# Performance work log

Measured on AMD Instinct MI355X. Metric: run time of the kernel, lower is better.

Reference implementation:

```python
import jax, jax.numpy as jnp
import numpy as np

NEG_SLOPE = 0.2


def setup_inputs() -> dict:
    key = jax.random.key(0)
    ks = jax.random.split(key, 7)
    N, E, IN, H, D = 100000, 1000000, 256, 4, 32
    feat = jax.random.normal(ks[0], (N, IN), dtype=jnp.float32)
    W_fc = jax.random.normal(ks[1], (H * D, IN), dtype=jnp.float32) * (1.0 / np.sqrt(IN))
    attn_l = jax.random.normal(ks[2], (1, H, D), dtype=jnp.float32) * 0.1
    attn_r = jax.random.normal(ks[3], (1, H, D), dtype=jnp.float32) * 0.1
    bias = jnp.zeros((H * D,), dtype=jnp.float32)
    src = jax.random.randint(ks[4], (E,), 0, N, dtype=jnp.int32)
    dst = jax.random.randint(ks[5], (E,), 0, N, dtype=jnp.int32)
    return {"feat": feat, "W_fc": W_fc, "attn_l": attn_l, "attn_r": attn_r, "bias": bias, "src": src, "dst": dst}


def reference(feat, W_fc, attn_l, attn_r, bias, src, dst):
    N = feat.shape[0]
    H, D = attn_l.shape[1], attn_l.shape[2]
    # fc projection; note: in the non-tuple path the module uses self.fc for
    # BOTH feat_src and feat_src2, so they are identical.
    h = (feat @ W_fc.T).reshape(N, H, D)  # [N,H,D]
    el = jnp.sum(h * attn_l, axis=-1)  # [N,H]
    er = jnpp_sum = jnp.sum(h * attn_r, axis=-1)  # [N,H]
    e = jax.nn.leaky_relu(el[src] + er[dst], NEG_SLOPE)  # [E,H]
    # edge softmax normalized over incoming edges of each dst node
    e_max = jax.ops.segment_max(e, dst, num_segments=N)  # [N,H]
    ex = jnp.exp(e - e_max[dst])
    denom = jax.ops.segment_sum(ex, dst, num_segments=N)  # [N,H]
    a = ex / denom[dst]  # [E,H]
    # attention-weighted aggregation: sum_e a_e * h[src_e] -> dst
    initial_ft = jax.ops.segment_sum(h[src] * a[:, :, None], dst, num_segments=N)
    # second path: u_mul_v then sum to dst (feat_src2 == feat_dst2 == h)
    add_ft = jax.ops.segment_sum(h[src] * h[dst], dst, num_segments=N)
    rst = initial_ft + add_ft + bias.reshape(1, H, D)
    return rst
```

## Files before the change

### kernel.cpp

```cpp
#include <hip/hip_runtime.h>
#include <hip/hip_bf16.h>
#include <hip/hip_fp16.h>
#include <math.h>

#define NEG_SLOPE 0.2f

typedef __attribute__((ext_vector_type(8))) short short8v;
typedef __attribute__((ext_vector_type(4))) float f32x4;

__device__ __forceinline__ float uas(unsigned int u) { return __uint_as_float(u); }

__device__ __forceinline__ unsigned short f2bf(float x) {
    __hip_bfloat16 b = __float2bfloat16(x);
    return *(unsigned short*)&b;
}

#define NPB_SHIFT 8
#define BCAP_SHIFT 13
#define BCAP (1 << BCAP_SHIFT)
#define BIN_EDGES 2048
#define BS_EPT    4
#define GEMM_BLOCKS 512

__global__ void k_prep(const float* __restrict__ W, const float* __restrict__ al,
                       const float* __restrict__ ar, short* __restrict__ wfrag,
                       int* __restrict__ bcur, int NB, int* __restrict__ tilectr) {
    int p = blockIdx.x * 256 + threadIdx.x;
    if (p < NB) bcur[p] = p << BCAP_SHIFT;
    if (p == 0) *tilectr = 0;
    if (p >= 144 * 32) return;
    int n = p >> 5, kg = p & 31;
    float v[8];
    if (n < 128) {
        const float* wp = W + (size_t)n * 256 + kg * 8;
        float4 v0 = *(const float4*)wp;
        float4 v1 = *(const float4*)(wp + 4);
        v[0] = v0.x; v[1] = v0.y; v[2] = v0.z; v[3] = v0.w;
        v[4] = v1.x; v[5] = v1.y; v[6] = v1.z; v[7] = v1.w;
    } else if (n < 136) {
        int i = n - 128, hh = i & 3, lr = i >> 2;
        const float* av = lr ? ar : al;
#pragma unroll
        for (int j = 0; j < 8; j++) v[j] = 0.f;
        for (int c = 0; c < 32; c++) {
            float a = av[hh * 32 + c];
            const float* wp = W + (size_t)(hh * 32 + c) * 256 + kg * 8;
#pragma unroll
            for (int j = 0; j < 8; j++) v[j] += a * wp[j];
        }
    } else {
#pragma unroll
        for (int j = 0; j < 8; j++) v[j] = 0.f;
    }
    short s8[8];
#pragma unroll
    for (int j = 0; j < 8; j++) s8[j] = (short)f2bf(v[j]);
    int kstep = kg >> 2, ntile = n >> 4;
    int L     = (kg & 3) * 16 + (n & 15);
    int slot  = kstep * 9 + ntile;
    *(short8v*)&wfrag[(slot * 64 + L) * 8] = *(short8v*)s8;
}

__global__ __launch_bounds__(512, 4) void k_gemm(const float* __restrict__ feat,
                                                 const short* __restrict__ wfrag,
                                                 unsigned short* __restrict__ hb,
                                                 float* __restrict__ el,
                                                 float* __restrict__ er, int N,
                                                 int ntiles,
                                                 int* __restrict__ tilectr) {
    __shared__ short wlds[36864];
    __shared__ int tsh;
    const int t    = threadIdx.x;
    const int lane = t & 63;
    const int wave = t >> 6;
    const int g    = lane >> 4;
    const int c    = lane & 15;

#pragma unroll
    for (int i = 0; i < 9; i++) {
        int p = t + i * 512;
        *(short8v*)&wlds[(size_t)p * 8] = *(const short8v*)&wfrag[(size_t)p * 8];
    }
    __syncthreads();

    for (;;) {
        if (t == 0) tsh = atomicAdd(tilectr, 1);
        __syncthreads();
        const int tile = tsh;
        __syncthreads();
        if (tile >= ntiles) break;

        const int n0  = tile * 128;
        const int row = n0 + wave * 16 + c;
        const int rc  = row < N ? row : N - 1;
        const float* ap = feat + (size_t)rc * 256 + g * 8;

        float4 a4[16];
#pragma unroll
        for (int ks = 0; ks < 8; ks++) {
            a4[2 * ks]     = *(const float4*)(ap + ks * 32);
            a4[2 * ks + 1] = *(const float4*)(ap + ks * 32 + 4);
        }

        f32x4 acc[9];
#pragma unroll
        for (int nt = 0; nt < 9; nt++) acc[nt] = (f32x4){0.f, 0.f, 0.f, 0.f};

#pragma unroll
        for (int ks = 0; ks < 8; ks++) {
            float4 v0 = a4[2 * ks], v1 = a4[2 * ks + 1];
            short s8[8];
            s8[0] = (short)f2bf(v0.x); s8[1] = (short)f2bf(v0.y);
            s8[2] = (short)f2bf(v0.z); s8[3] = (short)f2bf(v0.w);
            s8[4] = (short)f2bf(v1.x); s8[5] = (short)f2bf(v1.y);
            s8[6] = (short)f2bf(v1.z); s8[7] = (short)f2bf(v1.w);
            short8v afrag = *(short8v*)s8;
#pragma unroll
            for (int nt = 0; nt < 9; nt++) {
                short8v b = *(short8v*)&wlds[(((size_t)ks * 9 + nt) * 64 + lane) * 8];
                acc[nt] = __builtin_amdgcn_mfma_f32_16x16x32_bf16(afrag, b, acc[nt], 0, 0, 0);
            }
        }

#pragma unroll
        for (int r = 0; r < 4; r++) {
            int m = n0 + wave * 16 + g * 4 + r;
            if (m < N) {
#pragma unroll
                for (int nt = 0; nt < 8; nt++)
                    hb[(size_t)m * 128 + nt * 16 + c] = f2bf(acc[nt][r]);
                float av = acc[8][r];
                if (c < 4)      el[(size_t)m * 4 + c]       = av;
                else if (c < 8) er[(size_t)m * 4 + (c - 4)] = av;
            }
        }
    }
}

__global__ __launch_bounds__(512) void k_binscatter(const int* __restrict__ src,
                                                    const int* __restrict__ dst,
                                                    int* __restrict__ bcur,
                                                    unsigned int* __restrict__ binned,
                                                    int E, int NB) {
    __shared__ int hist[512];
    __shared__ int scn[512];
    __shared__ int lcur[512];
    __shared__ int gdelta[512];
    __shared__ int ebuf[BIN_EDGES];
    __shared__ int dbuf[BIN_EDGES];
    int t = threadIdx.x;
    hist[t] = 0;
    __syncthreads();
    int wbase = blockIdx.x * BIN_EDGES;
    int base  = wbase + t;
    int ne    = E - wbase; if (ne > BIN_EDGES) ne = BIN_EDGES;
    int sv[BS_EPT], dv[BS_EPT];
#pragma unroll
    for (int k = 0; k < BS_EPT; k++) {
        int idx = base + k * 512;
        if (idx < E) {
            sv[k] = src[idx];
            dv[k] = dst[idx];
            atomicAdd(&hist[dv[k] >> NPB_SHIFT], 1);
        } else {
            dv[k] = -1;
        }
    }
    __syncthreads();
    scn[t] = hist[t];
    __syncthreads();
    for (int off = 1; off < 512; off <<= 1) {
        int v = (t >= off) ? scn[t - off] : 0;
        __syncthreads();
        scn[t] += v;
        __syncthreads();
    }
    if (t < NB) {
        int h  = hist[t];
        int lb = scn[t] - h;
        int g  = h ? atomicAdd(&bcur[t], h) : 0;
        gdelta[t] = g - lb;
        lcur[t]   = lb;
    }
    __syncthreads();
#pragma unroll
    for (int k = 0; k < BS_EPT; k++) {
        if (dv[k] >= 0) {
            int bkt  = dv[k] >> NPB_SHIFT;
            int slot = atomicAdd(&lcur[bkt], 1);
            ebuf[slot] = sv[k];
            dbuf[slot] = dv[k];
        }
    }
    __syncthreads();
    for (int j = t; j < ne; j += 512) {
        int d = dbuf[j];
        binned[j + gdelta[d >> NPB_SHIFT]] =
            (unsigned int)ebuf[j] | ((unsigned int)(d & 255) << 24);
    }
}

__global__ __launch_bounds__(512) void k_csr(const unsigned int* __restrict__ binned,
                                             const int* __restrict__ bcur,
                                             int* __restrict__ startA,
                                             int* __restrict__ deg,
                                             int* __restrict__ src_csr, int N) {
    __shared__ int hist[256];
    __shared__ int scn[256];
    __shared__ int cur[256];
    __shared__ int sbuf[4096];
    int b = blockIdx.x;
    int t = threadIdx.x;
    int base = b << BCAP_SHIFT;
    int cnt  = bcur[b] - base;
    int node0 = b << NPB_SHIFT;
    if (t < 256) hist[t] = 0;
    __syncthreads();
    for (int i = t; i < cnt; i += 512) {
        unsigned int e = binned[base + i];
        atomicAdd(&hist[e >> 24], 1);
    }
    __syncthreads();
    int h = (t < 256) ? hist[t] : 0;
    if (t < 256) scn[t] = h;
    __syncthreads();
    for (int off = 1; off < 256; off <<= 1) {
        int v = (t < 256 && t >= off) ? scn[t - off] : 0;
        __syncthreads();
        if (t < 256) scn[t] += v;
        __syncthreads();
    }
    if (t < 256) {
        int excl  = scn[t] - h;
        int gnode = node0 + t;
        if (gnode < N) { startA[gnode] = base + excl; deg[gnode] = h; }
        cur[t] = excl;
    }
    __syncthreads();
    if (cnt <= 4096) {
        for (int i = t; i < cnt; i += 512) {
            unsigned int e = binned[base + i];
            int p = atomicAdd(&cur[e >> 24], 1);
            sbuf[p] = (int)(e & 0xFFFFFFu);
        }
        __syncthreads();
        for (int i = t; i < cnt; i += 512)
            src_csr[base + i] = sbuf[i];
    } else {
        for (int i = t; i < cnt; i += 512) {
            unsigned int e = binned[base + i];
            int p = atomicAdd(&cur[e >> 24], 1);
            src_csr[base + p] = (int)(e & 0xFFFFFFu);
        }
    }
}

__global__ __launch_bounds__(256) void k_agg(
        const unsigned int* __restrict__ hbu,
        const float* __restrict__ el, const float* __restrict__ er,
        const int* __restrict__ src_csr, const int* __restrict__ start,
        const int* __restrict__ deg,
        const float* __restrict__ bias, float* __restrict__ out, int N) {
    int wid  = blockIdx.x * 4 + (threadIdx.x >> 6);
    int lane = threadIdx.x & 63;
    if (wid >= N) return;
    int beg = __builtin_amdgcn_readfirstlane(start[wid]);
    int dg  = __builtin_amdgcn_readfirstlane(deg[wid]);
    int head = lane >> 4;

    float er_own = er[(size_t)wid * 4 + head];
    unsigned int uh = hbu[(size_t)wid * 64 + lane];
    float2 bv = ((const float2*)bias)[lane];

    float S1x = 0.f, S1y = 0.f, S2x = 0.f, S2y = 0.f, dd = 0.f;
    int i = 0;
    for (; i + 8 <= dg; i += 8) {
        int b = beg + i;
        int s[8];
#pragma unroll
        for (int k = 0; k < 8; k++) s[k] = src_csr[b + k];
        unsigned int u[8];
#pragma unroll
        for (int k = 0; k < 8; k++) u[k] = hbu[(size_t)s[k] * 64 + lane];
        float ev[8];
#pragma unroll
        for (int k = 0; k < 8; k++) ev[k] = el[(size_t)s[k] * 4 + head];
#pragma unroll
        for (int k = 0; k < 8; k++) {
            float tt = ev[k] + er_own;
            tt = fmaxf(tt, NEG_SLOPE * tt);
            float w = __expf(tt);
            float x = uas(u[k] << 16), y = uas(u[k] & 0xFFFF0000u);
            S1x += x; S1y += y;
            S2x += w * x; S2y += w * y;
            dd  += w;
        }
    }
    for (; i + 4 <= dg; i += 4) {
        int b = beg + i;
        int s[4];
#pragma unroll
        for (int k = 0; k < 4; k++) s[k] = src_csr[b + k];
        unsigned int u[4];
#pragma unroll
        for (int k = 0; k < 4; k++) u[k] = hbu[(size_t)s[k] * 64 + lane];
        float ev[4];
#pragma unroll
        for (int k = 0; k < 4; k++) ev[k] = el[(size_t)s[k] * 4 + head];
#pragma unroll
        for (int k = 0; k < 4; k++) {
            float tt = ev[k] + er_own;
            tt = fmaxf(tt, NEG_SLOPE * tt);
            float w = __expf(tt);
            float x = uas(u[k] << 16), y = uas(u[k] & 0xFFFF0000u);
            S1x += x; S1y += y;
            S2x += w * x; S2y += w * y;
            dd  += w;
        }
    }
    for (; i < dg; i++) {
        int s0 = src_csr[beg + i];
        unsigned int u0 = hbu[(size_t)s0 * 64 + lane];
        float tt = el[(size_t)s0 * 4 + head] + er_own;
        tt = fmaxf(tt, NEG_SLOPE * tt);
        float w0 = __expf(tt);
        float x0 = uas(u0 << 16), y0 = uas(u0 & 0xFFFF0000u);
        S1x += x0; S1y += y0;
        S2x += w0 * x0; S2y += w0 * y0;
        dd  += w0;
    }

    float hvx = uas(uh << 16), hvy = uas(uh & 0xFFFF0000u);
    float inv = dd > 0.f ? 1.f / dd : 0.f;
    float ox = bv.x + hvx * S1x + S2x * inv;
    float oy = bv.y + hvy * S1y + S2y * inv;
    float2 o = {ox, oy};
    ((float2*)(out + (size_t)wid * 128))[lane] = o;
}

extern "C" void kernel_launch(void* const* d_in, const int* in_sizes, int n_in,
                              void* d_out, int out_size, void* d_ws, size_t ws_size,
                              hipStream_t stream) {
    const float* feat = (const float*)d_in[0];
    const float* W_fc = (const float*)d_in[1];
    const float* al   = (const float*)d_in[2];
    const float* ar   = (const float*)d_in[3];
    const float* bias = (const float*)d_in[4];
    const int*   src  = (const int*)d_in[5];
    const int*   dst  = (const int*)d_in[6];
    const int N = in_sizes[0] / 256;
    const int E = in_sizes[5];
    const int NB = (N + 255) >> NPB_SHIFT;

    char* ws = (char*)d_ws;
    size_t off = 0;
    unsigned int* hbu = (unsigned int*)(ws + off); off += (size_t)N * 64 * 4;
    float* el         = (float*)(ws + off); off += (size_t)N * 4 * 4;
    float* er         = (float*)(ws + off); off += (size_t)N * 4 * 4;
    int* startA       = (int*)(ws + off);   off += (size_t)N * 4;
    int* deg          = (int*)(ws + off);   off += (size_t)N * 4;
    int* src_csr      = (int*)(ws + off);   off += (size_t)NB * BCAP * 4;
    unsigned int* binned = (unsigned int*)(ws + off); off += (size_t)NB * BCAP * 4;
    short* wfrag      = (short*)(ws + off); off += (size_t)72 * 64 * 8 * 2;
    int* bcur         = (int*)(ws + off);   off += 2048;
    int* tilectr      = (int*)(ws + off);   off += 256;

    float* out = (float*)d_out;

    int ntiles = (N + 127) / 128;
    int binWG  = (E + BIN_EDGES - 1) / BIN_EDGES;

    k_prep<<<18, 256, 0, stream>>>(W_fc, al, ar, wfrag, bcur, NB, tilectr);
    k_gemm<<<GEMM_BLOCKS, 512, 0, stream>>>(feat, wfrag, (unsigned short*)hbu,
                                            el, er, N, ntiles, tilectr);
    k_binscatter<<<binWG, 512, 0, stream>>>(src, dst, bcur, binned, E, NB);
    k_csr<<<NB, 512, 0, stream>>>(binned, bcur, startA, deg, src_csr, N);
    k_agg<<<(N + 3) / 4, 256, 0, stream>>>(hbu, el, er, src_csr, startA, deg,
                                           bias, out, N);
}
```

Baseline: 261.4 us.

## Fuse CSR construction and aggregation into one per-bucket LDS kernel

Replaces the separate CSR-build and aggregation kernels with one kernel. Each block takes half of a 256-node bucket, histograms and scatters the source ids into shared memory, then runs the same per-node aggregation with ids read from LDS. This removes the global src_csr/start/deg write-and-reread and one kernel launch. In exchange, each wave walks 16 nodes serially, each bucket's binned data is read by two blocks, and a bucket half with more than 3072 edges would read unwritten LDS.

```diff
diff --git a/kernel.cpp b/kernel.cpp
--- a/kernel.cpp
+++ b/kernel.cpp
@@ -21,6 +21,7 @@
 #define BIN_EDGES 2048
 #define BS_EPT    4
 #define GEMM_BLOCKS 512
+#define HCAP 3072
 
 __global__ void k_prep(const float* __restrict__ W, const float* __restrict__ al,
                        const float* __restrict__ ar, short* __restrict__ wfrag,
@@ -200,142 +201,132 @@
     }
 }
 
-__global__ __launch_bounds__(512) void k_csr(const unsigned int* __restrict__ binned,
-                                             const int* __restrict__ bcur,
-                                             int* __restrict__ startA,
-                                             int* __restrict__ deg,
-                                             int* __restrict__ src_csr, int N) {
-    __shared__ int hist[256];
-    __shared__ int scn[256];
-    __shared__ int cur[256];
-    __shared__ int sbuf[4096];
-    int b = blockIdx.x;
-    int t = threadIdx.x;
-    int base = b << BCAP_SHIFT;
-    int cnt  = bcur[b] - base;
-    int node0 = b << NPB_SHIFT;
-    if (t < 256) hist[t] = 0;
+__global__ __launch_bounds__(512) void k_csragg(
+        const unsigned int* __restrict__ binned, const int* __restrict__ bcur,
+        const unsigned int* __restrict__ hbu,
+        const float* __restrict__ el, const float* __restrict__ er,
+        const float* __restrict__ bias, float* __restrict__ out, int N) {
+    __shared__ int hist[128];
+    __shared__ int sstart[128];
+    __shared__ int cur[128];
+    __shared__ int sbuf[HCAP];
+    const int b    = blockIdx.x >> 1;
+    const int hh   = blockIdx.x & 1;
+    const int t    = threadIdx.x;
+    const int lane = t & 63;
+    const int wave = t >> 6;
+    const int base = b << BCAP_SHIFT;
+    const int cnt  = bcur[b] - base;
+    const int node0 = (b << NPB_SHIFT) + (hh << 7);
+
+    if (t < 128) hist[t] = 0;
     __syncthreads();
     for (int i = t; i < cnt; i += 512) {
         unsigned int e = binned[base + i];
-        atomicAdd(&hist[e >> 24], 1);
-    }
-    __syncthreads();
-    int h = (t < 256) ? hist[t] : 0;
-    if (t < 256) scn[t] = h;
-    __syncthreads();
-    for (int off = 1; off < 256; off <<= 1) {
-        int v = (t < 256 && t >= off) ? scn[t - off] : 0;
-        __syncthreads();
-        if (t < 256) scn[t] += v;
-        __syncthreads();
-    }
-    if (t < 256) {
-        int excl  = scn[t] - h;
-        int gnode = node0 + t;
-        if (gnode < N) { startA[gnode] = base + excl; deg[gnode] = h; }
-        cur[t] = excl;
-    }
-    __syncthreads();
-    if (cnt <= 4096) {
-        for (int i = t; i < cnt; i += 512) {
-            unsigned int e = binned[base + i];
-            int p = atomicAdd(&cur[e >> 24], 1);
-            sbuf[p] = (int)(e & 0xFFFFFFu);
-        }
-        __syncthreads();
-        for (int i = t; i < cnt; i += 512)
-            src_csr[base + i] = sbuf[i];
-    } else {
-        for (int i = t; i < cnt; i += 512) {
-            unsigned int e = binned[base + i];
-            int p = atomicAdd(&cur[e >> 24], 1);
-            src_csr[base + p] = (int)(e & 0xFFFFFFu);
-        }
-    }
-}
-
-__global__ __launch_bounds__(256) void k_agg(
-        const unsigned int* __restrict__ hbu,
-        const float* __restrict__ el, const float* __restrict__ er,
-        const int* __restrict__ src_csr, const int* __restrict__ start,
-        const int* __restrict__ deg,
-        const float* __restrict__ bias, float* __restrict__ out, int N) {
-    int wid  = blockIdx.x * 4 + (threadIdx.x >> 6);
-    int lane = threadIdx.x & 63;
-    if (wid >= N) return;
-    int beg = __builtin_amdgcn_readfirstlane(start[wid]);
-    int dg  = __builtin_amdgcn_readfirstlane(deg[wid]);
-    int head = lane >> 4;
-
-    float er_own = er[(size_t)wid * 4 + head];
-    unsigned int uh = hbu[(size_t)wid * 64 + lane];
+        int ld = e >> 24;
+        if ((ld >> 7) == hh) atomicAdd(&hist[ld & 127], 1);
+    }
+    __syncthreads();
+    int hv = (t < 128) ? hist[t] : 0;
+    if (t < 128) sstart[t] = hv;
+    __syncthreads();
+    for (int off = 1; off < 128; off <<= 1) {
+        int v = (t < 128 && t >= off) ? sstart[t - off] : 0;
+        __syncthreads();
+        if (t < 128) sstart[t] += v;
+        __syncthreads();
+    }
+    if (t < 128) {
+        int excl = sstart[t] - hv;
+        sstart[t] = excl;
+        cur[t]    = excl;
+    }
+    __syncthreads();
+    for (int i = t; i < cnt; i += 512) {
+        unsigned int e = binned[base + i];
+        int ld = e >> 24;
+        if ((ld >> 7) == hh) {
+            int p = atomicAdd(&cur[ld & 127], 1);
+            if (p < HCAP) sbuf[p] = (int)(e & 0xFFFFFFu);
+        }
+    }
+    __syncthreads();
+
+    const int head = lane >> 4;
     float2 bv = ((const float2*)bias)[lane];
-
-    float S1x = 0.f, S1y = 0.f, S2x = 0.f, S2y = 0.f, dd = 0.f;
-    int i = 0;
-    for (; i + 8 <= dg; i += 8) {
-        int b = beg + i;
-        int s[8];
-#pragma unroll
-        for (int k = 0; k < 8; k++) s[k] = src_csr[b + k];
-        unsigned int u[8];
-#pragma unroll
-        for (int k = 0; k < 8; k++) u[k] = hbu[(size_t)s[k] * 64 + lane];
-        float ev[8];
-#pragma unroll
-        for (int k = 0; k < 8; k++) ev[k] = el[(size_t)s[k] * 4 + head];
-#pragma unroll
-        for (int k = 0; k < 8; k++) {
-            float tt = ev[k] + er_own;
+    for (int j = 0; j < 16; j++) {
+        int ln    = wave * 16 + j;
+        int gnode = node0 + ln;
+        if (gnode >= N) break;
+        int beg = sstart[ln];
+        int dg  = hist[ln];
+
+        float er_own = er[(size_t)gnode * 4 + head];
+        unsigned int uh = hbu[(size_t)gnode * 64 + lane];
+
+        float S1x = 0.f, S1y = 0.f, S2x = 0.f, S2y = 0.f, dd = 0.f;
+        int i = 0;
+        for (; i + 8 <= dg; i += 8) {
+            int s[8];
+#pragma unroll
+            for (int k = 0; k < 8; k++) s[k] = sbuf[beg + i + k];
+            unsigned int u[8];
+#pragma unroll
+            for (int k = 0; k < 8; k++) u[k] = hbu[(size_t)s[k] * 64 + lane];
+            float ev[8];
+#pragma unroll
+            for (int k = 0; k < 8; k++) ev[k] = el[(size_t)s[k] * 4 + head];
+#pragma unroll
+            for (int k = 0; k < 8; k++) {
+                float tt = ev[k] + er_own;
+                tt = fmaxf(tt, NEG_SLOPE * tt);
+                float w = __expf(tt);
+                float x = uas(u[k] << 16), y = uas(u[k] & 0xFFFF0000u);
+                S1x += x; S1y += y;
+                S2x += w * x; S2y += w * y;
+                dd  += w;
+            }
+        }
+        for (; i + 4 <= dg; i += 4) {
+            int s[4];
+#pragma unroll
+            for (int k = 0; k < 4; k++) s[k] = sbuf[beg + i + k];
+            unsigned int u[4];
+#pragma unroll
+            for (int k = 0; k < 4; k++) u[k] = hbu[(size_t)s[k] * 64 + lane];
+            float ev[4];
+#pragma unroll
+            for (int k = 0; k < 4; k++) ev[k] = el[(size_t)s[k] * 4 + head];
+#pragma unroll
+            for (int k = 0; k < 4; k++) {
+                float tt = ev[k] + er_own;
+                tt = fmaxf(tt, NEG_SLOPE * tt);
+                float w = __expf(tt);
+                float x = uas(u[k] << 16), y = uas(u[k] & 0xFFFF0000u);
+                S1x += x; S1y += y;
+                S2x += w * x; S2y += w * y;
+                dd  += w;
+            }
+        }
+        for (; i < dg; i++) {
+            int s0 = sbuf[beg + i];
+            unsigned int u0 = hbu[(size_t)s0 * 64 + lane];
+            float tt = el[(size_t)s0 * 4 + head] + er_own;
             tt = fmaxf(tt, NEG_SLOPE * tt);
-            float w = __expf(tt);
-            float x = uas(u[k] << 16), y = uas(u[k] & 0xFFFF0000u);
-            S1x += x; S1y += y;
-            S2x += w * x; S2y += w * y;
-            dd  += w;
-        }
-    }
-    for (; i + 4 <= dg; i += 4) {
-        int b = beg + i;
-        int s[4];
-#pragma unroll
-        for (int k = 0; k < 4; k++) s[k] = src_csr[b + k];
-        unsigned int u[4];
-#pragma unroll
-        for (int k = 0; k < 4; k++) u[k] = hbu[(size_t)s[k] * 64 + lane];
-        float ev[4];
-#pragma unroll
-        for (int k = 0; k < 4; k++) ev[k] = el[(size_t)s[k] * 4 + head];
-#pragma unroll
-        for (int k = 0; k < 4; k++) {
-            float tt = ev[k] + er_own;
-            tt = fmaxf(tt, NEG_SLOPE * tt);
-            float w = __expf(tt);
-            float x = uas(u[k] << 16), y = uas(u[k] & 0xFFFF0000u);
-            S1x += x; S1y += y;
-            S2x += w * x; S2y += w * y;
-            dd  += w;
-        }
-    }
-    for (; i < dg; i++) {
-        int s0 = src_csr[beg + i];
-        unsigned int u0 = hbu[(size_t)s0 * 64 + lane];
-        float tt = el[(size_t)s0 * 4 + head] + er_own;
-        tt = fmaxf(tt, NEG_SLOPE * tt);
-        float w0 = __expf(tt);
-        float x0 = uas(u0 << 16), y0 = uas(u0 & 0xFFFF0000u);
-        S1x += x0; S1y += y0;
-        S2x += w0 * x0; S2y += w0 * y0;
-        dd  += w0;
-    }
-
-    float hvx = uas(uh << 16), hvy = uas(uh & 0xFFFF0000u);
-    float inv = dd > 0.f ? 1.f / dd : 0.f;
-    float ox = bv.x + hvx * S1x + S2x * inv;
-    float oy = bv.y + hvy * S1y + S2y * inv;
-    float2 o = {ox, oy};
-    ((float2*)(out + (size_t)wid * 128))[lane] = o;
+            float w0 = __expf(tt);
+            float x0 = uas(u0 << 16), y0 = uas(u0 & 0xFFFF0000u);
+            S1x += x0; S1y += y0;
+            S2x += w0 * x0; S2y += w0 * y0;
+            dd  += w0;
+        }
+
+        float hvx = uas(uh << 16), hvy = uas(uh & 0xFFFF0000u);
+        float inv = dd > 0.f ? 1.f / dd : 0.f;
+        float ox = bv.x + hvx * S1x + S2x * inv;
+        float oy = bv.y + hvy * S1y + S2y * inv;
+        float2 o = {ox, oy};
+        ((float2*)(out + (size_t)gnode * 128))[lane] = o;
+    }
 }
 
 extern "C" void kernel_launch(void* const* d_in, const int* in_sizes, int n_in,
@@ -357,9 +348,6 @@
     unsigned int* hbu = (unsigned int*)(ws + off); off += (size_t)N * 64 * 4;
     float* el         = (float*)(ws + off); off += (size_t)N * 4 * 4;
     float* er         = (float*)(ws + off); off += (size_t)N * 4 * 4;
-    int* startA       = (int*)(ws + off);   off += (size_t)N * 4;
-    int* deg          = (int*)(ws + off);   off += (size_t)N * 4;
-    int* src_csr      = (int*)(ws + off);   off += (size_t)NB * BCAP * 4;
     unsigned int* binned = (unsigned int*)(ws + off); off += (size_t)NB * BCAP * 4;
     short* wfrag      = (short*)(ws + off); off += (size_t)72 * 64 * 8 * 2;
     int* bcur         = (int*)(ws + off);   off += 2048;
@@ -374,7 +362,6 @@
     k_gemm<<<GEMM_BLOCKS, 512, 0, stream>>>(feat, wfrag, (unsigned short*)hbu,
                                             el, er, N, ntiles, tilectr);
     k_binscatter<<<binWG, 512, 0, stream>>>(src, dst, bcur, binned, E, NB);
-    k_csr<<<NB, 512, 0, stream>>>(binned, bcur, startA, deg, src_csr, N);
-    k_agg<<<(N + 3) / 4, 256, 0, stream>>>(hbu, el, er, src_csr, startA, deg,
-                                           bias, out, N);
-}
+    k_csragg<<<NB * 2, 512, 0, stream>>>(binned, bcur, hbu, el, er,
+                                         bias, out, N);
+}
```

Measured after the change: 270.0 us. +3.3%, slower.

## Stage A tile in swizzled LDS and split N columns across wave halves

Applied to the files above, without the earlier changes.

The projection GEMM now loads 64-row tiles of feat cooperatively with fully coalesced row reads, converts them to bf16 and stores them in XOR-swizzled shared memory. Each row group is handled by two waves, one computing four output column tiles and the other the remaining four plus the attention-logit tile. The atomic tile counter is replaced by a static grid-stride loop over 256 blocks. This aims to improve global-load coalescing and cut per-wave register pressure, at the cost of extra LDS traffic, barriers per tile, and a lower-occupancy launch.

```diff
diff --git a/kernel.cpp b/kernel.cpp
--- a/kernel.cpp
+++ b/kernel.cpp
@@ -20,14 +20,12 @@
 #define BCAP (1 << BCAP_SHIFT)
 #define BIN_EDGES 2048
 #define BS_EPT    4
-#define GEMM_BLOCKS 512
 
 __global__ void k_prep(const float* __restrict__ W, const float* __restrict__ al,
                        const float* __restrict__ ar, short* __restrict__ wfrag,
-                       int* __restrict__ bcur, int NB, int* __restrict__ tilectr) {
+                       int* __restrict__ bcur, int NB) {
     int p = blockIdx.x * 256 + threadIdx.x;
     if (p < NB) bcur[p] = p << BCAP_SHIFT;
-    if (p == 0) *tilectr = 0;
     if (p >= 144 * 32) return;
     int n = p >> 5, kg = p & 31;
     float v[8];
@@ -61,20 +59,21 @@
     *(short8v*)&wfrag[(slot * 64 + L) * 8] = *(short8v*)s8;
 }
 
-__global__ __launch_bounds__(512, 4) void k_gemm(const float* __restrict__ feat,
-                                                 const short* __restrict__ wfrag,
-                                                 unsigned short* __restrict__ hb,
-                                                 float* __restrict__ el,
-                                                 float* __restrict__ er, int N,
-                                                 int ntiles,
-                                                 int* __restrict__ tilectr) {
+__global__ __launch_bounds__(512) void k_gemm(const float* __restrict__ feat,
+                                              const short* __restrict__ wfrag,
+                                              unsigned short* __restrict__ hb,
+                                              float* __restrict__ el,
+                                              float* __restrict__ er, int N,
+                                              int ntiles) {
     __shared__ short wlds[36864];
-    __shared__ int tsh;
+    __shared__ short alds[16384];
     const int t    = threadIdx.x;
     const int lane = t & 63;
     const int wave = t >> 6;
     const int g    = lane >> 4;
     const int c    = lane & 15;
+    const int rg   = wave & 3;
+    const bool hiW = wave >= 4;
 
 #pragma unroll
     for (int i = 0; i < 9; i++) {
@@ -83,55 +82,76 @@
     }
     __syncthreads();
 
-    for (;;) {
-        if (t == 0) tsh = atomicAdd(tilectr, 1);
-        __syncthreads();
-        const int tile = tsh;
-        __syncthreads();
-        if (tile >= ntiles) break;
-
-        const int n0  = tile * 128;
-        const int row = n0 + wave * 16 + c;
-        const int rc  = row < N ? row : N - 1;
-        const float* ap = feat + (size_t)rc * 256 + g * 8;
-
-        float4 a4[16];
-#pragma unroll
-        for (int ks = 0; ks < 8; ks++) {
-            a4[2 * ks]     = *(const float4*)(ap + ks * 32);
-            a4[2 * ks + 1] = *(const float4*)(ap + ks * 32 + 4);
-        }
-
-        f32x4 acc[9];
-#pragma unroll
-        for (int nt = 0; nt < 9; nt++) acc[nt] = (f32x4){0.f, 0.f, 0.f, 0.f};
-
-#pragma unroll
-        for (int ks = 0; ks < 8; ks++) {
-            float4 v0 = a4[2 * ks], v1 = a4[2 * ks + 1];
-            short s8[8];
-            s8[0] = (short)f2bf(v0.x); s8[1] = (short)f2bf(v0.y);
-            s8[2] = (short)f2bf(v0.z); s8[3] = (short)f2bf(v0.w);
-            s8[4] = (short)f2bf(v1.x); s8[5] = (short)f2bf(v1.y);
-            s8[6] = (short)f2bf(v1.z); s8[7] = (short)f2bf(v1.w);
-            short8v afrag = *(short8v*)s8;
-#pragma unroll
-            for (int nt = 0; nt < 9; nt++) {
-                short8v b = *(short8v*)&wlds[(((size_t)ks * 9 + nt) * 64 + lane) * 8];
-                acc[nt] = __builtin_amdgcn_mfma_f32_16x16x32_bf16(afrag, b, acc[nt], 0, 0, 0);
+    char* abase = (char*)alds;
+
+    for (int tile = blockIdx.x; tile < ntiles; tile += gridDim.x) {
+        const int n0 = tile * 64;
+
+#pragma unroll
+        for (int p = 0; p < 8; p++) {
+            int rowl = p * 8 + wave;
+            int rc   = (n0 + rowl) < N ? (n0 + rowl) : N - 1;
+            float4 v = *(const float4*)(feat + (size_t)rc * 256 + lane * 4);
+            unsigned int lo = (unsigned int)f2bf(v.x) | ((unsigned int)f2bf(v.y) << 16);
+            unsigned int hi = (unsigned int)f2bf(v.z) | ((unsigned int)f2bf(v.w) << 16);
+            int byte = rowl * 512 + lane * 8;
+            byte ^= (rowl & 7) << 4;
+            *(uint2*)(abase + byte) = make_uint2(lo, hi);
+        }
+        __syncthreads();
+
+        const int rowl = rg * 16 + c;
+        const int aswz = (rowl & 7) << 4;
+        if (!hiW) {
+            f32x4 acc[4];
+#pragma unroll
+            for (int j = 0; j < 4; j++) acc[j] = (f32x4){0.f, 0.f, 0.f, 0.f};
+#pragma unroll
+            for (int ks = 0; ks < 8; ks++) {
+                int abyte = (rowl * 512 + ks * 64 + g * 16) ^ aswz;
+                short8v afrag = *(short8v*)(abase + abyte);
+#pragma unroll
+                for (int j = 0; j < 4; j++) {
+                    short8v b = *(short8v*)&wlds[(((size_t)ks * 9 + j) * 64 + lane) * 8];
+                    acc[j] = __builtin_amdgcn_mfma_f32_16x16x32_bf16(afrag, b, acc[j], 0, 0, 0);
+                }
             }
-        }
-
-#pragma unroll
-        for (int r = 0; r < 4; r++) {
-            int m = n0 + wave * 16 + g * 4 + r;
-            if (m < N) {
-#pragma unroll
-                for (int nt = 0; nt < 8; nt++)
-                    hb[(size_t)m * 128 + nt * 16 + c] = f2bf(acc[nt][r]);
-                float av = acc[8][r];
-                if (c < 4)      el[(size_t)m * 4 + c]       = av;
-                else if (c < 8) er[(size_t)m * 4 + (c - 4)] = av;
+            __syncthreads();
+#pragma unroll
+            for (int r = 0; r < 4; r++) {
+                int m = n0 + rg * 16 + g * 4 + r;
+                if (m < N) {
+#pragma unroll
+                    for (int j = 0; j < 4; j++)
+                        hb[(size_t)m * 128 + j * 16 + c] = f2bf(acc[j][r]);
+                }
+            }
+        } else {
+            f32x4 acc[5];
+#pragma unroll
+            for (int j = 0; j < 5; j++) acc[j] = (f32x4){0.f, 0.f, 0.f, 0.f};
+#pragma unroll
+            for (int ks = 0; ks < 8; ks++) {
+                int abyte = (rowl * 512 + ks * 64 + g * 16) ^ aswz;
+                short8v afrag = *(short8v*)(abase + abyte);
+#pragma unroll
+                for (int j = 0; j < 5; j++) {
+                    short8v b = *(short8v*)&wlds[(((size_t)ks * 9 + 4 + j) * 64 + lane) * 8];
+                    acc[j] = __builtin_amdgcn_mfma_f32_16x16x32_bf16(afrag, b, acc[j], 0, 0, 0);
+                }
+            }
+            __syncthreads();
+#pragma unroll
+            for (int r = 0; r < 4; r++) {
+                int m = n0 + rg * 16 + g * 4 + r;
+                if (m < N) {
+#pragma unroll
+                    for (int j = 0; j < 4; j++)
+                        hb[(size_t)m * 128 + (4 + j) * 16 + c] = f2bf(acc[j][r]);
+                    float av = acc[4][r];
+                    if (c < 4)      el[(size_t)m * 4 + c]       = av;
+                    else if (c < 8) er[(size_t)m * 4 + (c - 4)] = av;
+                }
             }
         }
     }
@@ -363,16 +383,15 @@
     unsigned int* binned = (unsigned int*)(ws + off); off += (size_t)NB * BCAP * 4;
     short* wfrag      = (short*)(ws + off); off += (size_t)72 * 64 * 8 * 2;
     int* bcur         = (int*)(ws + off);   off += 2048;
-    int* tilectr      = (int*)(ws + off);   off += 256;
 
     float* out = (float*)d_out;
 
-    int ntiles = (N + 127) / 128;
+    int ntiles = (N + 63) / 64;
     int binWG  = (E + BIN_EDGES - 1) / BIN_EDGES;
 
-    k_prep<<<18, 256, 0, stream>>>(W_fc, al, ar, wfrag, bcur, NB, tilectr);
-    k_gemm<<<GEMM_BLOCKS, 512, 0, stream>>>(feat, wfrag, (unsigned short*)hbu,
-                                            el, er, N, ntiles, tilectr);
+    k_prep<<<18, 256, 0, stream>>>(W_fc, al, ar, wfrag, bcur, NB);
+    k_gemm<<<256, 512, 0, stream>>>(feat, wfrag, (unsigned short*)hbu,
+                                    el, er, N, ntiles);
     k_binscatter<<<binWG, 512, 0, stream>>>(src, dst, bcur, binned, E, NB);
     k_csr<<<NB, 512, 0, stream>>>(binned, bcur, startA, deg, src_csr, N);
     k_agg<<<(N + 3) / 4, 256, 0, stream>>>(hbu, el, er, src_csr, startA, deg,
```

Measured after the change: 256.2 us. 1.02x faster.
